# Optimization experiments

Measured on AMD Instinct MI355X. Metric: run time of the kernel, lower is better.

## Reference

```python
import jax, jax.numpy as jnp
import numpy as np

N, D, P, NS = 2048, 64, 32, 512  # nnodes, stop_embedding_size, preference_dim, n_active_stops
LEAKY_SLOPE = 0.01
COS_EPS = 1e-8


def setup_inputs() -> dict:
    key = jax.random.key(0)
    ks = jax.random.split(key, 10)
    dist = jax.random.uniform(ks[0], (N, N), dtype=jnp.float32)
    stops = jax.random.randint(ks[1], (NS,), 0, N)
    emb_w = jax.random.normal(ks[2], (N, D), dtype=jnp.float32) * 0.05      # nn.Embedding weight
    lin_l_w = jax.random.normal(ks[3], (P, D), dtype=jnp.float32) * 0.05    # SAGEConv lin_l (aggregated)
    lin_l_b = jnp.zeros((P,), dtype=jnp.float32)
    lin_r_w = jax.random.normal(ks[4], (P, D), dtype=jnp.float32) * 0.05    # SAGEConv lin_r (root)
    edge_w = jax.random.normal(ks[5], (2 * P,), dtype=jnp.float32) * 0.05   # edge_summarizer weight
    edge_b = jnp.zeros((), dtype=jnp.float32)
    in_len = 2 * N + 3 + P
    comb_w = jax.random.normal(ks[6], (N, in_len), dtype=jnp.float32) * 0.02  # combiner weight
    comb_b = jnp.zeros((N,), dtype=jnp.float32)
    return {
        "dist": dist, "emb_w": emb_w,
        "lin_l_w": lin_l_w, "lin_l_b": lin_l_b, "lin_r_w": lin_r_w,
        "edge_w": edge_w, "edge_b": edge_b,
        "comb_w": comb_w, "comb_b": comb_b,
        "stops": stops, "weekday": 3, "vehicles": 5,
    }


def reference(dist, emb_w, lin_l_w, lin_l_b, lin_r_w, edge_w, edge_b,
              comb_w, comb_b, stops, weekday, vehicles):
    dt = emb_w.dtype
    # --- cosine-similarity graph build ---
    norm = jnp.maximum(jnp.linalg.norm(emb_w, axis=1, keepdims=True), COS_EPS)
    xn = emb_w / norm
    sim = xn @ xn.T                                   # [N, N]
    sim = sim * (1.0 - jnp.eye(N, dtype=dt))          # fill_diagonal_(0)
    keep = jnp.zeros((N,), dtype=bool).at[stops].set(True)
    adj = ((sim > 0.5) & keep[:, None] & keep[None, :]).astype(dt)  # [N, N]
    # --- SAGEConv (mean aggregation): lin_l(mean_j x_j) + lin_r(x_i) ---
    deg = jnp.maximum(adj.sum(axis=1, keepdims=True), 1.0)
    agg = (adj @ emb_w) / deg                         # [N, D]
    pref = agg @ lin_l_w.T + lin_l_b + emb_w @ lin_r_w.T   # [N, P]
    # --- all-pairs edge summaries: Linear([pref_i, pref_j]) + LeakyReLU ---
    # equivalent to concat-then-linear, without materializing [N^2, 2P]
    a = pref @ edge_w[:P]                             # [N]
    b = pref @ edge_w[P:]                             # [N]
    es = a[:, None] + b[None, :] + edge_b             # [N, N]
    es = jnp.where(es >= 0, es, LEAKY_SLOPE * es)
    # --- combiner + log-softmax ---
    weekday_feat = jnp.full((N, 1), weekday, dtype=dt)
    vehicle_feat = jnp.full((N, 1), vehicles, dtype=dt)
    stop_feat = keep.astype(dt)[:, None]
    combined = jnp.concatenate([pref, es, dist, weekday_feat, vehicle_feat, stop_feat], axis=1)
    out = combined @ comb_w.T + comb_b                # [N, N]
    return jax.nn.log_softmax(out, axis=1)
```

## Files before the change

kernel.cpp:

```cpp
#include <hip/hip_runtime.h>

typedef unsigned short u16;
typedef __attribute__((ext_vector_type(8))) short bf16x8;
typedef __attribute__((ext_vector_type(4))) float f32x4;

__device__ __forceinline__ u16 f2bf(float f) {
    return (u16)((__float_as_uint(f) + 0x8000u) >> 16);
}

#define N_NODES 2048
#define D_EMB 64
#define P_DIM 32
#define NS_STOPS 512
#define IN_LEN 4131
#define NKT 65

#define SWZ(row, c) ((((row) * 8) + ((c) ^ ((row) & 7))) * 8)

__device__ __forceinline__ void gload16(const u16* g, u16* l) {
    __builtin_amdgcn_global_load_lds((const __attribute__((address_space(1))) void*)g,
                                     (__attribute__((address_space(3))) void*)l, 16, 0, 0);
}

__global__ __launch_bounds__(256) void k_aggpref(const float* __restrict__ emb, const int* __restrict__ stops,
                                                 const float* __restrict__ lin_l_w, const float* __restrict__ lin_l_b,
                                                 const float* __restrict__ lin_r_w, const float* __restrict__ edge_w,
                                                 float* __restrict__ pref, float* __restrict__ av, float* __restrict__ bv,
                                                 float* __restrict__ keepf) {
    __shared__ int bm[64];
    __shared__ int kl[NS_STOPS];
    __shared__ float xiS[8][D_EMB];
    __shared__ float aggS[8][D_EMB];
    __shared__ float niS[8];
    __shared__ int degS[8];
    __shared__ int kiS[8];
    __shared__ int cnt;
    int t = threadIdx.x;
    int i0 = blockIdx.x * 8;
    if (t < 64) bm[t] = 0;
    if (t == 0) cnt = 0;
    if (t < 8) degS[t] = 0;
    ((float*)aggS)[t] = 0.f;
    ((float*)aggS)[t + 256] = 0.f;
    __syncthreads();
    {
        int s0 = stops[t], s1 = stops[t + 256];
        atomicOr(&bm[s0 >> 5], 1 << (s0 & 31));
        atomicOr(&bm[s1 >> 5], 1 << (s1 & 31));
    }
    __syncthreads();
    {
        int w = bm[t >> 2];
        int base = (t >> 2) * 32 + (t & 3) * 8;
        #pragma unroll
        for (int e = 0; e < 8; ++e)
            if ((w >> ((t & 3) * 8 + e)) & 1) { int p = atomicAdd(&cnt, 1); kl[p] = base + e; }
    }
    if (t < 8) { int i = i0 + t; kiS[t] = (bm[i >> 5] >> (i & 31)) & 1; }
    {
        int n = t >> 5, d = (t & 31) * 2;
        xiS[n][d]     = emb[(i0 + n) * D_EMB + d];
        xiS[n][d + 1] = emb[(i0 + n) * D_EMB + d + 1];
    }
    __syncthreads();
    if (t < 8) {
        float s = 0.f;
        #pragma unroll
        for (int d = 0; d < D_EMB; ++d) s += xiS[t][d] * xiS[t][d];
        niS[t] = fmaxf(sqrtf(s), 1e-8f);
    }
    __syncthreads();
    int nk = cnt;
    for (int u = t; u < nk; u += 256) {
        int j = kl[u];
        const f32x4* ej = (const f32x4*)&emb[j * D_EMB];
        f32x4 er[16];
        f32x4 sv = {0.f, 0.f, 0.f, 0.f};
        #pragma unroll
        for (int d = 0; d < 16; ++d) { er[d] = ej[d]; sv += er[d] * er[d]; }
        float nj = fmaxf(sqrtf(sv[0] + sv[1] + sv[2] + sv[3]), 1e-8f);
        #pragma unroll
        for (int n = 0; n < 8; ++n) {
            if (!kiS[n] || j == i0 + n) continue;
            f32x4 dv = {0.f, 0.f, 0.f, 0.f};
            #pragma unroll
            for (int d = 0; d < 16; ++d) dv += (*(const f32x4*)&xiS[n][d * 4]) * er[d];
            float dot = dv[0] + dv[1] + dv[2] + dv[3];
            if (dot > 0.5f * niS[n] * nj) {
                atomicAdd(&degS[n], 1);
                #pragma unroll
                for (int d = 0; d < 16; ++d) {
                    atomicAdd(&aggS[n][d * 4 + 0], er[d][0]);
                    atomicAdd(&aggS[n][d * 4 + 1], er[d][1]);
                    atomicAdd(&aggS[n][d * 4 + 2], er[d][2]);
                    atomicAdd(&aggS[n][d * 4 + 3], er[d][3]);
                }
            }
        }
    }
    __syncthreads();
    {
        int n = t >> 5, p = t & 31;
        int i = i0 + n;
        float inv = kiS[n] ? (1.f / fmaxf((float)degS[n], 1.0f)) : 0.f;
        float s = lin_l_b[p];
        const float* wl = &lin_l_w[p * D_EMB];
        const float* wr = &lin_r_w[p * D_EMB];
        #pragma unroll
        for (int d = 0; d < D_EMB; ++d) s += aggS[n][d] * inv * wl[d] + xiS[n][d] * wr[d];
        pref[i * P_DIM + p] = s;
        float a = s * edge_w[p];
        float b = s * edge_w[P_DIM + p];
        #pragma unroll
        for (int off = 16; off; off >>= 1) { a += __shfl_xor(a, off, 32); b += __shfl_xor(b, off, 32); }
        if (p == 0) { av[i] = a; bv[i] = b; keepf[i] = (float)kiS[n]; }
    }
}

__global__ __launch_bounds__(256) void k_pack(const float* __restrict__ comb_w, const float* __restrict__ comb_b,
                                              const int* __restrict__ wk_p, const int* __restrict__ vh_p,
                                              const float* __restrict__ dist, const float* __restrict__ pref,
                                              const float* __restrict__ av, const float* __restrict__ bv,
                                              const float* __restrict__ edge_b,
                                              u16* __restrict__ Bp, u16* __restrict__ Ap,
                                              float* __restrict__ cvec, float* __restrict__ w3) {
    int kt = blockIdx.x;
    int ty = blockIdx.y;
    int t = threadIdx.x;
    if (ty < 16) {
        int nt = ty;
        u16* tb = Bp + ((size_t)nt * NKT + kt) * 8192;
        #pragma unroll
        for (int it = 0; it < 4; ++it) {
            int q = t + it * 256;
            int r = q >> 3, c = q & 7;
            int j = nt * 128 + r;
            int k0 = kt * 64 + c * 8;
            const float* cw = comb_w + (size_t)j * IN_LEN;
            bf16x8 v;
            if (k0 < 4096) {
                f32x4 f0, f1;
                __builtin_memcpy(&f0, cw + 32 + k0, 16);
                __builtin_memcpy(&f1, cw + 36 + k0, 16);
                #pragma unroll
                for (int e = 0; e < 4; ++e) { v[e] = (short)f2bf(f0[e]); v[4 + e] = (short)f2bf(f1[e]); }
            } else if (k0 < 4128) {
                f32x4 f0, f1;
                __builtin_memcpy(&f0, cw + (k0 - 4096), 16);
                __builtin_memcpy(&f1, cw + (k0 - 4092), 16);
                #pragma unroll
                for (int e = 0; e < 4; ++e) { v[e] = (short)f2bf(f0[e]); v[4 + e] = (short)f2bf(f1[e]); }
            } else {
                #pragma unroll
                for (int e = 0; e < 8; ++e) v[e] = 0;
            }
            *(bf16x8*)&tb[r * 64 + ((c ^ (r & 7)) * 8)] = v;
        }
        if (kt == 64 && t < 128) {
            int j = nt * 128 + t;
            const float* cw = comb_w + (size_t)j * IN_LEN;
            float wk = (float)wk_p[0], vh = (float)vh_p[0];
            cvec[j] = wk * cw[4128] + vh * cw[4129] + comb_b[j];
            w3[j] = cw[4130];
        }
    } else {
        int rt = ty - 16;
        u16* ta = Ap + ((size_t)rt * NKT + kt) * 4096;
        float eb = edge_b[0];
        #pragma unroll
        for (int it = 0; it < 2; ++it) {
            int q = t + it * 256;
            int r = q >> 3, c = q & 7;
            int row = rt * 64 + r;
            int k0 = kt * 64 + c * 8;
            bf16x8 v;
            if (k0 < 2048) {
                float ab = av[row] + eb;
                f32x4 f0 = *(const f32x4*)(bv + k0);
                f32x4 f1 = *(const f32x4*)(bv + k0 + 4);
                #pragma unroll
                for (int e = 0; e < 4; ++e) {
                    float s0 = ab + f0[e]; s0 = (s0 >= 0.f) ? s0 : 0.01f * s0;
                    float s1 = ab + f1[e]; s1 = (s1 >= 0.f) ? s1 : 0.01f * s1;
                    v[e] = (short)f2bf(s0); v[4 + e] = (short)f2bf(s1);
                }
            } else if (k0 < 4096) {
                const f32x4* dp = (const f32x4*)(dist + (size_t)row * 2048 + (k0 - 2048));
                f32x4 f0 = dp[0], f1 = dp[1];
                #pragma unroll
                for (int e = 0; e < 4; ++e) { v[e] = (short)f2bf(f0[e]); v[4 + e] = (short)f2bf(f1[e]); }
            } else if (k0 < 4128) {
                const f32x4* pp = (const f32x4*)(pref + (size_t)row * P_DIM + (k0 - 4096));
                f32x4 f0 = pp[0], f1 = pp[1];
                #pragma unroll
                for (int e = 0; e < 4; ++e) { v[e] = (short)f2bf(f0[e]); v[4 + e] = (short)f2bf(f1[e]); }
            } else {
                #pragma unroll
                for (int e = 0; e < 8; ++e) v[e] = 0;
            }
            *(bf16x8*)&ta[r * 64 + ((c ^ (r & 7)) * 8)] = v;
        }
    }
}

__global__ __launch_bounds__(256, 4) void k_gemm_d(const u16* __restrict__ Ap, const u16* __restrict__ Bp,
                                                   const float* __restrict__ cvec, const float* __restrict__ w3,
                                                   const float* __restrict__ keepf,
                                                   float* __restrict__ Cout) {
    __shared__ __attribute__((aligned(16))) short As[2][4096];
    __shared__ __attribute__((aligned(16))) short Bs[2][4096];
    int t = threadIdx.x;
    int b = blockIdx.x;
    int c = b & 7, u = b >> 3;
    int mt = (c & 1) * 16 + (u & 15);
    int nt = (c >> 1) * 8 + (u >> 4);
    int tileM = mt * 64, tileN = nt * 64;
    int lane = t & 63;
    int wid = t >> 6;
    int waveM = wid & 1, waveN = wid >> 1;
    int l16 = lane & 15, quad = lane >> 4;

    f32x4 acc[2][2];
    #pragma unroll
    for (int a_ = 0; a_ < 2; ++a_)
        #pragma unroll
        for (int b_ = 0; b_ < 2; ++b_) acc[a_][b_] = (f32x4){0.f, 0.f, 0.f, 0.f};

    const u16* gA = Ap + ((size_t)mt * NKT) * 4096 + t * 8;
    const u16* gB = Bp + ((size_t)(nt >> 1) * NKT) * 8192 + (nt & 1) * 4096 + t * 8;

#define ISSUE(ktv, bb) do { \
        const u16* a0 = gA + (size_t)(ktv) * 4096; \
        const u16* b0 = gB + (size_t)(ktv) * 8192; \
        u16* ad = (u16*)As[bb] + t * 8; \
        u16* bd = (u16*)Bs[bb] + t * 8; \
        gload16(a0, ad); \
        gload16(a0 + 2048, ad + 2048); \
        gload16(b0, bd); \
        gload16(b0 + 2048, bd + 2048); \
    } while (0)

    ISSUE(0, 0);

    int cur = 0;
    for (int kt = 0; kt < NKT; ++kt) {
        __syncthreads();
        if (kt + 1 < NKT) ISSUE(kt + 1, cur ^ 1);
        const short* Asc = As[cur];
        const short* Bsc = Bs[cur];
        #pragma unroll
        for (int kk = 0; kk < 64; kk += 32) {
            int cbase = kk >> 3;
            bf16x8 af[2], bfr[2];
            #pragma unroll
            for (int mi = 0; mi < 2; ++mi) {
                int row = waveM * 32 + mi * 16 + l16;
                af[mi] = *(const bf16x8*)&Asc[SWZ(row, cbase + quad)];
            }
            #pragma unroll
            for (int ni = 0; ni < 2; ++ni) {
                int row = waveN * 32 + ni * 16 + l16;
                bfr[ni] = *(const bf16x8*)&Bsc[SWZ(row, cbase + quad)];
            }
            #pragma unroll
            for (int mi = 0; mi < 2; ++mi)
                #pragma unroll
                for (int ni = 0; ni < 2; ++ni)
                    acc[mi][ni] = __builtin_amdgcn_mfma_f32_16x16x32_bf16(af[mi], bfr[ni], acc[mi][ni], 0, 0, 0);
        }
        cur ^= 1;
    }
#undef ISSUE
    #pragma unroll
    for (int mi = 0; mi < 2; ++mi)
        #pragma unroll
        for (int ni = 0; ni < 2; ++ni) {
            int row0 = tileM + waveM * 32 + mi * 16 + quad * 4;
            int col = tileN + waveN * 32 + ni * 16 + l16;
            float cv = cvec[col], wv = w3[col];
            float* cp = Cout + (size_t)row0 * N_NODES + col;
            #pragma unroll
            for (int rr = 0; rr < 4; ++rr)
                cp[(size_t)rr * N_NODES] = acc[mi][ni][rr] + cv + keepf[row0 + rr] * wv;
        }
}

__global__ __launch_bounds__(256) void k_epi(float* __restrict__ out) {
    int i = blockIdx.x, t = threadIdx.x;
    __shared__ float redmax[4], redsum[4];
    f32x4* orow = (f32x4*)(out + (size_t)i * N_NODES);
    f32x4 v0 = orow[t];
    f32x4 v1 = orow[t + 256];
    float vmax = fmaxf(fmaxf(fmaxf(v0[0], v0[1]), fmaxf(v0[2], v0[3])),
                       fmaxf(fmaxf(v1[0], v1[1]), fmaxf(v1[2], v1[3])));
    #pragma unroll
    for (int off = 32; off; off >>= 1) vmax = fmaxf(vmax, __shfl_xor(vmax, off, 64));
    if ((t & 63) == 0) redmax[t >> 6] = vmax;
    __syncthreads();
    vmax = fmaxf(fmaxf(redmax[0], redmax[1]), fmaxf(redmax[2], redmax[3]));
    float se = 0.f;
    #pragma unroll
    for (int e = 0; e < 4; ++e) se += expf(v0[e] - vmax) + expf(v1[e] - vmax);
    #pragma unroll
    for (int off = 32; off; off >>= 1) se += __shfl_xor(se, off, 64);
    if ((t & 63) == 0) redsum[t >> 6] = se;
    __syncthreads();
    se = redsum[0] + redsum[1] + redsum[2] + redsum[3];
    float lz = vmax + logf(se);
    orow[t] = v0 - lz;
    orow[t + 256] = v1 - lz;
}

extern "C" void kernel_launch(void* const* d_in, const int* in_sizes, int n_in,
                              void* d_out, int out_size, void* d_ws, size_t ws_size,
                              hipStream_t stream) {
    const float* dist    = (const float*)d_in[0];
    const float* emb     = (const float*)d_in[1];
    const float* lin_l_w = (const float*)d_in[2];
    const float* lin_l_b = (const float*)d_in[3];
    const float* lin_r_w = (const float*)d_in[4];
    const float* edge_w  = (const float*)d_in[5];
    const float* edge_b  = (const float*)d_in[6];
    const float* comb_w  = (const float*)d_in[7];
    const float* comb_b  = (const float*)d_in[8];
    const int* stops     = (const int*)d_in[9];
    const int* wk        = (const int*)d_in[10];
    const int* vh        = (const int*)d_in[11];

    char* ws = (char*)d_ws;
    float* pref  = (float*)(ws + 0);
    float* av    = (float*)(ws + 262144);
    float* bv    = (float*)(ws + 270336);
    float* cvec  = (float*)(ws + 278528);
    float* w3    = (float*)(ws + 286720);
    float* keepf = (float*)(ws + 294912);
    u16*   Ap    = (u16*)(ws + 303104);
    u16*   Bp    = (u16*)(ws + 17342464);
    float* out   = (float*)d_out;

    hipLaunchKernelGGL(k_aggpref, dim3(256),    dim3(256), 0, stream, emb, stops,
                       lin_l_w, lin_l_b, lin_r_w, edge_w, pref, av, bv, keepf);
    hipLaunchKernelGGL(k_pack,    dim3(65, 48), dim3(256), 0, stream, comb_w, comb_b, wk, vh,
                       dist, pref, av, bv, edge_b, Bp, Ap, cvec, w3);
    hipLaunchKernelGGL(k_gemm_d,  dim3(1024),   dim3(256), 0, stream, Ap, Bp, cvec, w3, keepf, out);
    hipLaunchKernelGGL(k_epi,     dim3(2048),   dim3(256), 0, stream, out);
}
```

Before: 184.8 us.

## Overlap aggregation/pref with independent weight and dist packing in one launch

Merges the graph-aggregation/pref kernel with the packing of comb_w (B operand) and the dist part of the A operand into one launch, since those do not depend on pref. Only the tiles that need pref/av/bv (edge-summary and pref columns) are packed by a new small follow-up kernel. The goal is to overlap the latency-bound aggregation blocks with bandwidth-bound packing and shorten the serial chain. The cost is a larger mixed-role grid and one extra launch.

```diff
diff --git a/kernel.cpp b/kernel.cpp
--- a/kernel.cpp
+++ b/kernel.cpp
@@ -22,11 +22,16 @@
                                      (__attribute__((address_space(3))) void*)l, 16, 0, 0);
 }
 
-__global__ __launch_bounds__(256) void k_aggpref(const float* __restrict__ emb, const int* __restrict__ stops,
-                                                 const float* __restrict__ lin_l_w, const float* __restrict__ lin_l_b,
-                                                 const float* __restrict__ lin_r_w, const float* __restrict__ edge_w,
-                                                 float* __restrict__ pref, float* __restrict__ av, float* __restrict__ bv,
-                                                 float* __restrict__ keepf) {
+__global__ __launch_bounds__(256) void k_front(const float* __restrict__ emb, const int* __restrict__ stops,
+                                               const float* __restrict__ lin_l_w, const float* __restrict__ lin_l_b,
+                                               const float* __restrict__ lin_r_w, const float* __restrict__ edge_w,
+                                               const float* __restrict__ comb_w, const float* __restrict__ comb_b,
+                                               const int* __restrict__ wk_p, const int* __restrict__ vh_p,
+                                               const float* __restrict__ dist,
+                                               float* __restrict__ pref, float* __restrict__ av, float* __restrict__ bv,
+                                               float* __restrict__ keepf,
+                                               u16* __restrict__ Bp, u16* __restrict__ Ap,
+                                               float* __restrict__ cvec, float* __restrict__ w3) {
     __shared__ int bm[64];
     __shared__ int kl[NS_STOPS];
     __shared__ float xiS[8][D_EMB];
@@ -36,99 +41,90 @@
     __shared__ int kiS[8];
     __shared__ int cnt;
     int t = threadIdx.x;
-    int i0 = blockIdx.x * 8;
-    if (t < 64) bm[t] = 0;
-    if (t == 0) cnt = 0;
-    if (t < 8) degS[t] = 0;
-    ((float*)aggS)[t] = 0.f;
-    ((float*)aggS)[t + 256] = 0.f;
-    __syncthreads();
-    {
-        int s0 = stops[t], s1 = stops[t + 256];
-        atomicOr(&bm[s0 >> 5], 1 << (s0 & 31));
-        atomicOr(&bm[s1 >> 5], 1 << (s1 & 31));
-    }
-    __syncthreads();
-    {
-        int w = bm[t >> 2];
-        int base = (t >> 2) * 32 + (t & 3) * 8;
-        #pragma unroll
-        for (int e = 0; e < 8; ++e)
-            if ((w >> ((t & 3) * 8 + e)) & 1) { int p = atomicAdd(&cnt, 1); kl[p] = base + e; }
-    }
-    if (t < 8) { int i = i0 + t; kiS[t] = (bm[i >> 5] >> (i & 31)) & 1; }
-    {
-        int n = t >> 5, d = (t & 31) * 2;
-        xiS[n][d]     = emb[(i0 + n) * D_EMB + d];
-        xiS[n][d + 1] = emb[(i0 + n) * D_EMB + d + 1];
-    }
-    __syncthreads();
-    if (t < 8) {
-        float s = 0.f;
-        #pragma unroll
-        for (int d = 0; d < D_EMB; ++d) s += xiS[t][d] * xiS[t][d];
-        niS[t] = fmaxf(sqrtf(s), 1e-8f);
-    }
-    __syncthreads();
-    int nk = cnt;
-    for (int u = t; u < nk; u += 256) {
-        int j = kl[u];
-        const f32x4* ej = (const f32x4*)&emb[j * D_EMB];
-        f32x4 er[16];
-        f32x4 sv = {0.f, 0.f, 0.f, 0.f};
-        #pragma unroll
-        for (int d = 0; d < 16; ++d) { er[d] = ej[d]; sv += er[d] * er[d]; }
-        float nj = fmaxf(sqrtf(sv[0] + sv[1] + sv[2] + sv[3]), 1e-8f);
-        #pragma unroll
-        for (int n = 0; n < 8; ++n) {
-            if (!kiS[n] || j == i0 + n) continue;
-            f32x4 dv = {0.f, 0.f, 0.f, 0.f};
-            #pragma unroll
-            for (int d = 0; d < 16; ++d) dv += (*(const f32x4*)&xiS[n][d * 4]) * er[d];
-            float dot = dv[0] + dv[1] + dv[2] + dv[3];
-            if (dot > 0.5f * niS[n] * nj) {
-                atomicAdd(&degS[n], 1);
-                #pragma unroll
-                for (int d = 0; d < 16; ++d) {
-                    atomicAdd(&aggS[n][d * 4 + 0], er[d][0]);
-                    atomicAdd(&aggS[n][d * 4 + 1], er[d][1]);
-                    atomicAdd(&aggS[n][d * 4 + 2], er[d][2]);
-                    atomicAdd(&aggS[n][d * 4 + 3], er[d][3]);
+    int b = blockIdx.x;
+    if (b < 256) {
+        int i0 = b * 8;
+        if (t < 64) bm[t] = 0;
+        if (t == 0) cnt = 0;
+        if (t < 8) degS[t] = 0;
+        ((float*)aggS)[t] = 0.f;
+        ((float*)aggS)[t + 256] = 0.f;
+        __syncthreads();
+        {
+            int s0 = stops[t], s1 = stops[t + 256];
+            atomicOr(&bm[s0 >> 5], 1 << (s0 & 31));
+            atomicOr(&bm[s1 >> 5], 1 << (s1 & 31));
+        }
+        __syncthreads();
+        {
+            int w = bm[t >> 2];
+            int base = (t >> 2) * 32 + (t & 3) * 8;
+            #pragma unroll
+            for (int e = 0; e < 8; ++e)
+                if ((w >> ((t & 3) * 8 + e)) & 1) { int p = atomicAdd(&cnt, 1); kl[p] = base + e; }
+        }
+        if (t < 8) { int i = i0 + t; kiS[t] = (bm[i >> 5] >> (i & 31)) & 1; }
+        {
+            int n = t >> 5, d = (t & 31) * 2;
+            xiS[n][d]     = emb[(i0 + n) * D_EMB + d];
+            xiS[n][d + 1] = emb[(i0 + n) * D_EMB + d + 1];
+        }
+        __syncthreads();
+        if (t < 8) {
+            float s = 0.f;
+            #pragma unroll
+            for (int d = 0; d < D_EMB; ++d) s += xiS[t][d] * xiS[t][d];
+            niS[t] = fmaxf(sqrtf(s), 1e-8f);
+        }
+        __syncthreads();
+        int nk = cnt;
+        for (int u = t; u < nk; u += 256) {
+            int j = kl[u];
+            const f32x4* ej = (const f32x4*)&emb[j * D_EMB];
+            f32x4 er[16];
+            f32x4 sv = {0.f, 0.f, 0.f, 0.f};
+            #pragma unroll
+            for (int d = 0; d < 16; ++d) { er[d] = ej[d]; sv += er[d] * er[d]; }
+            float nj = fmaxf(sqrtf(sv[0] + sv[1] + sv[2] + sv[3]), 1e-8f);
+            #pragma unroll
+            for (int n = 0; n < 8; ++n) {
+                if (!kiS[n] || j == i0 + n) continue;
+                f32x4 dv = {0.f, 0.f, 0.f, 0.f};
+                #pragma unroll
+                for (int d = 0; d < 16; ++d) dv += (*(const f32x4*)&xiS[n][d * 4]) * er[d];
+                float dot = dv[0] + dv[1] + dv[2] + dv[3];
+                if (dot > 0.5f * niS[n] * nj) {
+                    atomicAdd(&degS[n], 1);
+                    #pragma unroll
+                    for (int d = 0; d < 16; ++d) {
+                        atomicAdd(&aggS[n][d * 4 + 0], er[d][0]);
+                        atomicAdd(&aggS[n][d * 4 + 1], er[d][1]);
+                        atomicAdd(&aggS[n][d * 4 + 2], er[d][2]);
+                        atomicAdd(&aggS[n][d * 4 + 3], er[d][3]);
+                    }
                 }
             }
         }
-    }
-    __syncthreads();
-    {
-        int n = t >> 5, p = t & 31;
-        int i = i0 + n;
-        float inv = kiS[n] ? (1.f / fmaxf((float)degS[n], 1.0f)) : 0.f;
-        float s = lin_l_b[p];
-        const float* wl = &lin_l_w[p * D_EMB];
-        const float* wr = &lin_r_w[p * D_EMB];
-        #pragma unroll
-        for (int d = 0; d < D_EMB; ++d) s += aggS[n][d] * inv * wl[d] + xiS[n][d] * wr[d];
-        pref[i * P_DIM + p] = s;
-        float a = s * edge_w[p];
-        float b = s * edge_w[P_DIM + p];
-        #pragma unroll
-        for (int off = 16; off; off >>= 1) { a += __shfl_xor(a, off, 32); b += __shfl_xor(b, off, 32); }
-        if (p == 0) { av[i] = a; bv[i] = b; keepf[i] = (float)kiS[n]; }
-    }
-}
-
-__global__ __launch_bounds__(256) void k_pack(const float* __restrict__ comb_w, const float* __restrict__ comb_b,
-                                              const int* __restrict__ wk_p, const int* __restrict__ vh_p,
-                                              const float* __restrict__ dist, const float* __restrict__ pref,
-                                              const float* __restrict__ av, const float* __restrict__ bv,
-                                              const float* __restrict__ edge_b,
-                                              u16* __restrict__ Bp, u16* __restrict__ Ap,
-                                              float* __restrict__ cvec, float* __restrict__ w3) {
-    int kt = blockIdx.x;
-    int ty = blockIdx.y;
-    int t = threadIdx.x;
-    if (ty < 16) {
-        int nt = ty;
+        __syncthreads();
+        {
+            int n = t >> 5, p = t & 31;
+            int i = i0 + n;
+            float inv = kiS[n] ? (1.f / fmaxf((float)degS[n], 1.0f)) : 0.f;
+            float s = lin_l_b[p];
+            const float* wl = &lin_l_w[p * D_EMB];
+            const float* wr = &lin_r_w[p * D_EMB];
+            #pragma unroll
+            for (int d = 0; d < D_EMB; ++d) s += aggS[n][d] * inv * wl[d] + xiS[n][d] * wr[d];
+            pref[i * P_DIM + p] = s;
+            float a = s * edge_w[p];
+            float bb = s * edge_w[P_DIM + p];
+            #pragma unroll
+            for (int off = 16; off; off >>= 1) { a += __shfl_xor(a, off, 32); bb += __shfl_xor(bb, off, 32); }
+            if (p == 0) { av[i] = a; bv[i] = bb; keepf[i] = (float)kiS[n]; }
+        }
+    } else if (b < 1296) {
+        int bq = b - 256;
+        int nt = bq / 65, kt = bq % 65;
         u16* tb = Bp + ((size_t)nt * NKT + kt) * 8192;
         #pragma unroll
         for (int it = 0; it < 4; ++it) {
@@ -164,42 +160,62 @@
             w3[j] = cw[4130];
         }
     } else {
-        int rt = ty - 16;
+        int bq = b - 1296;
+        int rt = bq >> 5, kt = 32 + (bq & 31);
         u16* ta = Ap + ((size_t)rt * NKT + kt) * 4096;
-        float eb = edge_b[0];
         #pragma unroll
         for (int it = 0; it < 2; ++it) {
             int q = t + it * 256;
             int r = q >> 3, c = q & 7;
             int row = rt * 64 + r;
             int k0 = kt * 64 + c * 8;
+            const f32x4* dp = (const f32x4*)(dist + (size_t)row * 2048 + (k0 - 2048));
+            f32x4 f0 = dp[0], f1 = dp[1];
             bf16x8 v;
-            if (k0 < 2048) {
-                float ab = av[row] + eb;
-                f32x4 f0 = *(const f32x4*)(bv + k0);
-                f32x4 f1 = *(const f32x4*)(bv + k0 + 4);
-                #pragma unroll
-                for (int e = 0; e < 4; ++e) {
-                    float s0 = ab + f0[e]; s0 = (s0 >= 0.f) ? s0 : 0.01f * s0;
-                    float s1 = ab + f1[e]; s1 = (s1 >= 0.f) ? s1 : 0.01f * s1;
-                    v[e] = (short)f2bf(s0); v[4 + e] = (short)f2bf(s1);
-                }
-            } else if (k0 < 4096) {
-                const f32x4* dp = (const f32x4*)(dist + (size_t)row * 2048 + (k0 - 2048));
-                f32x4 f0 = dp[0], f1 = dp[1];
-                #pragma unroll
-                for (int e = 0; e < 4; ++e) { v[e] = (short)f2bf(f0[e]); v[4 + e] = (short)f2bf(f1[e]); }
-            } else if (k0 < 4128) {
-                const f32x4* pp = (const f32x4*)(pref + (size_t)row * P_DIM + (k0 - 4096));
-                f32x4 f0 = pp[0], f1 = pp[1];
-                #pragma unroll
-                for (int e = 0; e < 4; ++e) { v[e] = (short)f2bf(f0[e]); v[4 + e] = (short)f2bf(f1[e]); }
-            } else {
-                #pragma unroll
-                for (int e = 0; e < 8; ++e) v[e] = 0;
-            }
+            #pragma unroll
+            for (int e = 0; e < 4; ++e) { v[e] = (short)f2bf(f0[e]); v[4 + e] = (short)f2bf(f1[e]); }
             *(bf16x8*)&ta[r * 64 + ((c ^ (r & 7)) * 8)] = v;
         }
+    }
+}
+
+__global__ __launch_bounds__(256) void k_packA2(const float* __restrict__ pref,
+                                                const float* __restrict__ av, const float* __restrict__ bv,
+                                                const float* __restrict__ edge_b,
+                                                u16* __restrict__ Ap) {
+    int b = blockIdx.x;
+    int rt = b / 33, kti = b % 33;
+    int kt = (kti < 32) ? kti : 64;
+    int t = threadIdx.x;
+    u16* ta = Ap + ((size_t)rt * NKT + kt) * 4096;
+    float eb = edge_b[0];
+    #pragma unroll
+    for (int it = 0; it < 2; ++it) {
+        int q = t + it * 256;
+        int r = q >> 3, c = q & 7;
+        int row = rt * 64 + r;
+        int k0 = kt * 64 + c * 8;
+        bf16x8 v;
+        if (k0 < 2048) {
+            float ab = av[row] + eb;
+            f32x4 f0 = *(const f32x4*)(bv + k0);
+            f32x4 f1 = *(const f32x4*)(bv + k0 + 4);
+            #pragma unroll
+            for (int e = 0; e < 4; ++e) {
+                float s0 = ab + f0[e]; s0 = (s0 >= 0.f) ? s0 : 0.01f * s0;
+                float s1 = ab + f1[e]; s1 = (s1 >= 0.f) ? s1 : 0.01f * s1;
+                v[e] = (short)f2bf(s0); v[4 + e] = (short)f2bf(s1);
+            }
+        } else if (k0 < 4128) {
+            const f32x4* pp = (const f32x4*)(pref + (size_t)row * P_DIM + (k0 - 4096));
+            f32x4 f0 = pp[0], f1 = pp[1];
+            #pragma unroll
+            for (int e = 0; e < 4; ++e) { v[e] = (short)f2bf(f0[e]); v[4 + e] = (short)f2bf(f1[e]); }
+        } else {
+            #pragma unroll
+            for (int e = 0; e < 8; ++e) v[e] = 0;
+        }
+        *(bf16x8*)&ta[r * 64 + ((c ^ (r & 7)) * 8)] = v;
     }
 }
 
@@ -338,10 +354,10 @@
     u16*   Bp    = (u16*)(ws + 17342464);
     float* out   = (float*)d_out;
 
-    hipLaunchKernelGGL(k_aggpref, dim3(256),    dim3(256), 0, stream, emb, stops,
-                       lin_l_w, lin_l_b, lin_r_w, edge_w, pref, av, bv, keepf);
-    hipLaunchKernelGGL(k_pack,    dim3(65, 48), dim3(256), 0, stream, comb_w, comb_b, wk, vh,
-                       dist, pref, av, bv, edge_b, Bp, Ap, cvec, w3);
-    hipLaunchKernelGGL(k_gemm_d,  dim3(1024),   dim3(256), 0, stream, Ap, Bp, cvec, w3, keepf, out);
-    hipLaunchKernelGGL(k_epi,     dim3(2048),   dim3(256), 0, stream, out);
-}
+    hipLaunchKernelGGL(k_front,  dim3(2320), dim3(256), 0, stream, emb, stops,
+                       lin_l_w, lin_l_b, lin_r_w, edge_w, comb_w, comb_b, wk, vh,
+                       dist, pref, av, bv, keepf, Bp, Ap, cvec, w3);
+    hipLaunchKernelGGL(k_packA2, dim3(1056), dim3(256), 0, stream, pref, av, bv, edge_b, Ap);
+    hipLaunchKernelGGL(k_gemm_d, dim3(1024), dim3(256), 0, stream, Ap, Bp, cvec, w3, keepf, out);
+    hipLaunchKernelGGL(k_epi,    dim3(2048), dim3(256), 0, stream, out);
+}
```

Result: faster. 175.7 us (-4.9%).
